# Kernel optimization log

Measured on AMD Instinct MI355X. Metric: run time of the kernel, lower is better.

Reference implementation:

```python
import jax, jax.numpy as jnp
import numpy as np

N, INV, M, K, H = 131072, 256, 256, 64, 512
EPS = 1e-6  # rms norm eps
LN_EPS = 1e-5  # torch LayerNorm default


def setup_inputs() -> dict:
    key = jax.random.key(0)
    ks = jax.random.split(key, 12)
    r = lambda i, shp, s=1.0: jax.random.normal(ks[i], shp, jnp.float32) * s
    return {
        "atomic_embeddings": r(0, (N, INV + 3 * M)),
        "mean_inv": r(1, (INV,)) * 0.1,
        "std_inv": jax.random.uniform(ks[2], (INV,), jnp.float32, 0.5, 1.5),
        "rms_gamma": jnp.ones((M,), jnp.float32),
        "W0": r(3, (M, K)),
        "W1": r(4, (M, K)),
        "W2": r(5, (M, K)),
        "w_cross": r(6, (K, K)),
        "w_dot": r(7, (K, K)),
        "ln_w": jnp.ones((K,), jnp.float32),
        "ln_b": jnp.zeros((K,), jnp.float32),
        "g_w1": r(8, (INV, H)) / np.sqrt(INV),
        "g_b1": jnp.zeros((H,), jnp.float32),
        "g_w2": r(9, (H, K)) / np.sqrt(H),
        "g_b2": jnp.zeros((K,), jnp.float32),
    }


def reference(atomic_embeddings, mean_inv, std_inv, rms_gamma, W0, W1, W2,
              w_cross, w_dot, ln_w, ln_b, g_w1, g_b1, g_w2, g_b2):
    # split invariants (0e scalars come first) / equivariants (1o vectors)
    inv = atomic_embeddings[:, :INV]                       # [N, INV]
    eq = atomic_embeddings[:, INV:].reshape(-1, M, 3)      # [N, M, 3] e3nn (mul, ir) layout

    # rescale invariants
    inv = (inv - mean_inv) / std_inv

    # equivariant RMS layer norm over the M irrep channels (norm-based)
    n2 = jnp.sum(eq * eq, axis=-1)                          # [N, M] squared vector norms
    rms = jnp.sqrt(jnp.mean(n2, axis=-1, keepdims=True) + EPS)  # [N, 1]
    eq = eq * (rms_gamma / rms)[..., None]                  # [N, M, 3]

    # o3.Linear Mx1o -> Kx1o (per-component GEMM, e3nn 1/sqrt(fan_in) path norm)
    s_lin = 1.0 / np.sqrt(M)
    x0 = jnp.einsum('nmi,mk->nki', eq, W0) * s_lin          # [N, K, 3]
    x1 = jnp.einsum('nmi,mk->nki', eq, W1) * s_lin
    x2 = jnp.einsum('nmi,mk->nki', eq, W2) * s_lin

    # tp_cross: Kx1o (x) Kx1o -> Kx1e, 'uvu' weighted, component norm.
    # CG(1,1->1) = eps_ijk/sqrt(6); path weight sqrt(dim(1e)/fan_in)=sqrt(3/K)
    # => overall 1/sqrt(2K). Contract weight into x1 first to stay O(N K^2).
    y1 = jnp.einsum('nvj,uv->nuj', x1, w_cross)             # [N, K, 3]
    cross = jnp.cross(x0, y1) / np.sqrt(2.0 * K)            # [N, K, 3] (1e)

    # tp_dot: Kx1e (x) Kx1o -> Kx0o, 'uvu' weighted, component norm.
    # CG(1,1->0) = delta_ij/sqrt(3); path weight sqrt(1/K) => 1/sqrt(3K).
    y2 = jnp.einsum('nvj,uv->nuj', x2, w_dot)               # [N, K, 3]
    chi = jnp.sum(cross * y2, axis=-1) / np.sqrt(3.0 * K)   # [N, K] pseudoscalars

    # LayerNorm over K
    mu = jnp.mean(chi, axis=-1, keepdims=True)
    var = jnp.mean(jnp.square(chi - mu), axis=-1, keepdims=True)
    out = (chi - mu) / jnp.sqrt(var + LN_EPS) * ln_w + ln_b

    # ChiGate: sigmoid(Linear(SiLU(Linear(inv))))
    gate = jax.nn.sigmoid(jax.nn.silu(inv @ g_w1 + g_b1) @ g_w2 + g_b2)
    return gate * out
```

## Files before the change

kernel.cpp:

```cpp
#include <hip/hip_runtime.h>
#include <math.h>

#define ROW_D 1024
#define INV_D 256

typedef short bf16x8 __attribute__((ext_vector_type(8)));
typedef float f32x4 __attribute__((ext_vector_type(4)));

#define MFMA16(a,b,c) __builtin_amdgcn_mfma_f32_16x16x32_bf16((a),(b),(c),0,0,0)

__device__ __forceinline__ unsigned short f2bf(float f) {
    union { float f; unsigned int u; } x; x.f = f;
    return (unsigned short)((x.u + 0x7FFFu + ((x.u >> 16) & 1u)) >> 16);
}
__device__ __forceinline__ float bf2f(unsigned short h) {
    union { unsigned int u; float f; } x; x.u = ((unsigned int)h) << 16;
    return x.f;
}

__global__ void prep_kernel(
    const float* __restrict__ g_w1, const float* __restrict__ mean_inv,
    const float* __restrict__ std_inv, const float* __restrict__ g_w2,
    const float* __restrict__ W0, const float* __restrict__ W1,
    const float* __restrict__ W2, const float* __restrict__ rms_gamma,
    const float* __restrict__ w_cross, const float* __restrict__ w_dot,
    const float* __restrict__ g_b1,
    unsigned short* __restrict__ W1t, unsigned short* __restrict__ W2t,
    unsigned short* __restrict__ Wcat, unsigned short* __restrict__ wcb,
    unsigned short* __restrict__ wdb, float* __restrict__ b1p)
{
    const int nth = gridDim.x * 256;
    for (int idx = blockIdx.x * 256 + threadIdx.x; idx < 221696; idx += nth) {
        if (idx < 131072) {
            int h = idx >> 8, m = idx & 255;
            W1t[idx] = f2bf(g_w1[m * 512 + h] / std_inv[m]);
        } else if (idx < 163840) {
            int t = idx - 131072; int k = t >> 9, h = t & 511;
            W2t[t] = f2bf(g_w2[h * 64 + k]);
        } else if (idx < 212992) {
            int t = idx - 163840; int r = t >> 8, m = t & 255;
            int tt = r >> 6, k = r & 63;
            const float* Wt = (tt == 0) ? W0 : ((tt == 1) ? W1 : W2);
            Wcat[t] = f2bf(Wt[m * 64 + k] * rms_gamma[m] * 0.0625f);
        } else if (idx < 217088) {
            int t = idx - 212992; wcb[t] = f2bf(w_cross[t]);
        } else if (idx < 221184) {
            int t = idx - 217088; wdb[t] = f2bf(w_dot[t]);
        } else {
            int h = idx - 221184;
            float s = 0.f;
            for (int m = 0; m < 256; ++m)
                s += mean_inv[m] / std_inv[m] * g_w1[m * 512 + h];
            b1p[h] = g_b1[h] - s;
        }
    }
}

__global__ __launch_bounds__(256, 3) void gate_kernel(
    const float* __restrict__ emb,
    const unsigned short* __restrict__ W1t,
    const unsigned short* __restrict__ W2t,
    const float* __restrict__ b1p,
    const float* __restrict__ g_b2,
    float* __restrict__ out)
{
    __shared__ __align__(16) char smem[43008];
    unsigned short* As   = (unsigned short*)smem;
    unsigned short* acts = (unsigned short*)(smem + 33792);

    const int tid = threadIdx.x;
    const int wv = tid >> 6, ln = tid & 63;
    const int lr = ln & 15, lq = ln >> 4;
    const int wr = (wv & 1) << 1;
    const int wc = (wv >> 1) << 1;
    const long n0 = (long)blockIdx.x * 64;

#pragma unroll
    for (int i = 0; i < 16; ++i) {
        int idx = tid + i * 256;
        int atom = idx >> 6;
        int c4 = (idx & 63) << 2;
        float4 v = *(const float4*)(emb + (n0 + atom) * ROW_D + c4);
        ushort4 h;
        h.x = f2bf(v.x); h.y = f2bf(v.y); h.z = f2bf(v.z); h.w = f2bf(v.w);
        *(ushort4*)&As[atom * 264 + c4] = h;
    }
    __syncthreads();

    f32x4 acc2[2][2];
#pragma unroll
    for (int r = 0; r < 2; ++r)
#pragma unroll
        for (int c = 0; c < 2; ++c) acc2[r][c] = (f32x4){0.f, 0.f, 0.f, 0.f};

    for (int hc = 0; hc < 8; ++hc) {
        f32x4 acc1[2][2];
#pragma unroll
        for (int r = 0; r < 2; ++r)
#pragma unroll
            for (int c = 0; c < 2; ++c) acc1[r][c] = (f32x4){0.f, 0.f, 0.f, 0.f};

#pragma unroll
        for (int ks = 0; ks < 8; ++ks) {
            bf16x8 af[2], bf[2];
#pragma unroll
            for (int r = 0; r < 2; ++r)
                af[r] = *(const bf16x8*)&As[((wr + r) * 16 + lr) * 264 + ks * 32 + lq * 8];
#pragma unroll
            for (int c = 0; c < 2; ++c)
                bf[c] = *(const bf16x8*)(W1t + (hc * 64 + (wc + c) * 16 + lr) * 256
                                              + ks * 32 + lq * 8);
#pragma unroll
            for (int r = 0; r < 2; ++r)
#pragma unroll
                for (int c = 0; c < 2; ++c)
                    acc1[r][c] = MFMA16(af[r], bf[c], acc1[r][c]);
        }

#pragma unroll
        for (int c = 0; c < 2; ++c) {
            int hl = (wc + c) * 16 + lr;
            float b = b1p[hc * 64 + hl];
#pragma unroll
            for (int r = 0; r < 2; ++r)
#pragma unroll
                for (int g = 0; g < 4; ++g) {
                    int atom = (wr + r) * 16 + lq * 4 + g;
                    float v = acc1[r][c][g] + b;
                    acts[atom * 72 + hl] = f2bf(v / (1.f + __expf(-v)));
                }
        }
        __syncthreads();

#pragma unroll
        for (int ks = 0; ks < 2; ++ks) {
            bf16x8 af[2], bf[2];
#pragma unroll
            for (int r = 0; r < 2; ++r)
                af[r] = *(const bf16x8*)&acts[((wr + r) * 16 + lr) * 72 + ks * 32 + lq * 8];
#pragma unroll
            for (int c = 0; c < 2; ++c)
                bf[c] = *(const bf16x8*)(W2t + ((wc + c) * 16 + lr) * 512
                                              + hc * 64 + ks * 32 + lq * 8);
#pragma unroll
            for (int r = 0; r < 2; ++r)
#pragma unroll
                for (int c = 0; c < 2; ++c)
                    acc2[r][c] = MFMA16(af[r], bf[c], acc2[r][c]);
        }
        __syncthreads();
    }

#pragma unroll
    for (int c = 0; c < 2; ++c) {
        int k = (wc + c) * 16 + lr;
        float b2v = g_b2[k];
#pragma unroll
        for (int r = 0; r < 2; ++r)
#pragma unroll
            for (int g = 0; g < 4; ++g) {
                int atom = (wr + r) * 16 + lq * 4 + g;
                float v = acc2[r][c][g] + b2v;
                out[(n0 + atom) * 64 + k] = 1.f / (1.f + __expf(-v));
            }
    }
}

__global__ __launch_bounds__(256, 3) void chi_kernel(
    const float* __restrict__ emb,
    const unsigned short* __restrict__ Wcat,
    const unsigned short* __restrict__ wcb,
    const unsigned short* __restrict__ wdb,
    const float* __restrict__ ln_w,
    const float* __restrict__ ln_b,
    float* __restrict__ out)
{
    __shared__ __align__(16) char smem[49024];
    unsigned short* Aeq = (unsigned short*)smem;
    unsigned short* Xl1 = (unsigned short*)smem;
    unsigned short* Xl2 = (unsigned short*)(smem + 13824);
    unsigned short* y1l = (unsigned short*)smem;
    unsigned short* y2l = (unsigned short*)(smem + 13824);
    unsigned short* x0l = (unsigned short*)(smem + 27648);
    float* chi_s = (float*)(smem + 40192);
    float* rms_s = (float*)(smem + 48640);
    float* mu_s  = (float*)(smem + 48768);
    float* isd_s = (float*)(smem + 48896);

    const int tid = threadIdx.x;
    const int wv = tid >> 6, ln = tid & 63;
    const int lr = ln & 15, lq = ln >> 4;
    const int a_t = tid >> 3, st = tid & 7;
    const long n0 = (long)blockIdx.x * 32;

    f32x4 acc[6][3];
#pragma unroll
    for (int tr = 0; tr < 6; ++tr)
#pragma unroll
        for (int c = 0; c < 3; ++c) acc[tr][c] = (f32x4){0.f, 0.f, 0.f, 0.f};
    float sumsq = 0.f;

    for (int half = 0; half < 2; ++half) {
        if (half) __syncthreads();
#pragma unroll
        for (int g = 0; g < 4; ++g) {
            int m0 = st * 16 + g * 4;
            int mg = half * 128 + m0;
            const float* p = emb + (n0 + a_t) * ROW_D + INV_D + (long)mg * 3;
            float4 v0 = *(const float4*)(p);
            float4 v1 = *(const float4*)(p + 4);
            float4 v2 = *(const float4*)(p + 8);
            sumsq += v0.x * v0.x + v0.y * v0.y + v0.z * v0.z + v0.w * v0.w
                   + v1.x * v1.x + v1.y * v1.y + v1.z * v1.z + v1.w * v1.w
                   + v2.x * v2.x + v2.y * v2.y + v2.z * v2.z + v2.w * v2.w;
            ushort4 h0, h1, h2;
            h0.x = f2bf(v0.x); h0.y = f2bf(v0.w); h0.z = f2bf(v1.z); h0.w = f2bf(v2.y);
            h1.x = f2bf(v0.y); h1.y = f2bf(v1.x); h1.z = f2bf(v1.w); h1.w = f2bf(v2.z);
            h2.x = f2bf(v0.z); h2.y = f2bf(v1.y); h2.z = f2bf(v2.x); h2.w = f2bf(v2.w);
            *(ushort4*)&Aeq[(0 * 32 + a_t) * 136 + m0] = h0;
            *(ushort4*)&Aeq[(1 * 32 + a_t) * 136 + m0] = h1;
            *(ushort4*)&Aeq[(2 * 32 + a_t) * 136 + m0] = h2;
        }
        __syncthreads();
#pragma unroll
        for (int ks = 0; ks < 4; ++ks) {
            bf16x8 bfr[3];
#pragma unroll
            for (int c = 0; c < 3; ++c)
                bfr[c] = *(const bf16x8*)(Wcat + ((wv * 3 + c) * 16 + lr) * 256
                                               + half * 128 + ks * 32 + lq * 8);
#pragma unroll
            for (int tr = 0; tr < 6; ++tr) {
                bf16x8 af = *(const bf16x8*)&Aeq[(tr * 16 + lr) * 136 + ks * 32 + lq * 8];
#pragma unroll
                for (int c = 0; c < 3; ++c)
                    acc[tr][c] = MFMA16(af, bfr[c], acc[tr][c]);
            }
        }
    }
    sumsq += __shfl_xor(sumsq, 1);
    sumsq += __shfl_xor(sumsq, 2);
    sumsq += __shfl_xor(sumsq, 4);
    if (st == 0) rms_s[a_t] = rsqrtf(sumsq * (1.f / 256.f) + 1e-6f);
    __syncthreads();

    float rmv[2][4];
#pragma unroll
    for (int p = 0; p < 2; ++p)
#pragma unroll
        for (int g = 0; g < 4; ++g) rmv[p][g] = rms_s[p * 16 + lq * 4 + g];

#pragma unroll
    for (int tr = 0; tr < 6; ++tr)
#pragma unroll
        for (int c = 0; c < 3; ++c) {
            int colg = (wv * 3 + c) * 16 + lr;
            int t = colg >> 6, k = colg & 63;
#pragma unroll
            for (int g = 0; g < 4; ++g) {
                int rowg = tr * 16 + lq * 4 + g;
                int ii = rowg >> 5, atom = rowg & 31;
                unsigned short hb = f2bf(acc[tr][c][g] * rmv[tr & 1][g]);
                if (t == 0)      x0l[atom * 196 + k * 3 + ii] = hb;
                else if (t == 1) Xl1[(atom * 3 + ii) * 72 + k] = hb;
                else             Xl2[(atom * 3 + ii) * 72 + k] = hb;
            }
        }
    __syncthreads();

    const int ts = wv & 1, cp = wv >> 1;
    const unsigned short* Xs = ts ? Xl2 : Xl1;
    const unsigned short* Wg = ts ? wdb : wcb;
    f32x4 yacc[6][2];
#pragma unroll
    for (int tr = 0; tr < 6; ++tr)
#pragma unroll
        for (int c = 0; c < 2; ++c) yacc[tr][c] = (f32x4){0.f, 0.f, 0.f, 0.f};
#pragma unroll
    for (int ks = 0; ks < 2; ++ks) {
        bf16x8 bfr[2];
#pragma unroll
        for (int c = 0; c < 2; ++c)
            bfr[c] = *(const bf16x8*)(Wg + ((cp * 2 + c) * 16 + lr) * 64 + ks * 32 + lq * 8);
#pragma unroll
        for (int tr = 0; tr < 6; ++tr) {
            bf16x8 af = *(const bf16x8*)&Xs[(tr * 16 + lr) * 72 + ks * 32 + lq * 8];
#pragma unroll
            for (int c = 0; c < 2; ++c)
                yacc[tr][c] = MFMA16(af, bfr[c], yacc[tr][c]);
        }
    }
    __syncthreads();

    unsigned short* Yd = ts ? y2l : y1l;
#pragma unroll
    for (int tr = 0; tr < 6; ++tr)
#pragma unroll
        for (int c = 0; c < 2; ++c) {
            int u = (cp * 2 + c) * 16 + lr;
#pragma unroll
            for (int g = 0; g < 4; ++g) {
                int rowg = tr * 16 + lq * 4 + g;
                Yd[rowg * 72 + u] = f2bf(yacc[tr][c][g]);
            }
        }
    __syncthreads();

    const float CHI_SCALE = 1.0f / sqrtf(24576.0f);
#pragma unroll
    for (int q = 0; q < 8; ++q) {
        int u = st + 8 * q;
        float x0a = bf2f(x0l[a_t * 196 + u * 3 + 0]);
        float x0b = bf2f(x0l[a_t * 196 + u * 3 + 1]);
        float x0c = bf2f(x0l[a_t * 196 + u * 3 + 2]);
        float y1a = bf2f(y1l[(a_t * 3 + 0) * 72 + u]);
        float y1b = bf2f(y1l[(a_t * 3 + 1) * 72 + u]);
        float y1c = bf2f(y1l[(a_t * 3 + 2) * 72 + u]);
        float y2a = bf2f(y2l[(a_t * 3 + 0) * 72 + u]);
        float y2b = bf2f(y2l[(a_t * 3 + 1) * 72 + u]);
        float y2c = bf2f(y2l[(a_t * 3 + 2) * 72 + u]);
        float c0 = x0b * y1c - x0c * y1b;
        float c1 = x0c * y1a - x0a * y1c;
        float c2 = x0a * y1b - x0b * y1a;
        chi_s[a_t * 66 + u] = (c0 * y2a + c1 * y2b + c2 * y2c) * CHI_SCALE;
    }
    __syncthreads();

    float s = 0.f;
#pragma unroll
    for (int q = 0; q < 8; ++q) s += chi_s[a_t * 66 + st + 8 * q];
    s += __shfl_xor(s, 1); s += __shfl_xor(s, 2); s += __shfl_xor(s, 4);
    float mu = s * (1.f / 64.f);
    float vv = 0.f;
#pragma unroll
    for (int q = 0; q < 8; ++q) {
        float d = chi_s[a_t * 66 + st + 8 * q] - mu;
        vv += d * d;
    }
    vv += __shfl_xor(vv, 1); vv += __shfl_xor(vv, 2); vv += __shfl_xor(vv, 4);
    if (st == 0) {
        mu_s[a_t]  = mu;
        isd_s[a_t] = rsqrtf(vv * (1.f / 64.f) + 1e-5f);
    }
    __syncthreads();

    float lw = ln_w[ln], lb = ln_b[ln];
#pragma unroll
    for (int aa = 0; aa < 8; ++aa) {
        int atom = wv * 8 + aa;
        float val = (chi_s[atom * 66 + ln] - mu_s[atom]) * isd_s[atom] * lw + lb;
        long o = (n0 + atom) * 64 + ln;
        out[o] = out[o] * val;
    }
}

extern "C" void kernel_launch(void* const* d_in, const int* in_sizes, int n_in,
                              void* d_out, int out_size, void* d_ws, size_t ws_size,
                              hipStream_t stream)
{
    const float* emb       = (const float*)d_in[0];
    const float* mean_inv  = (const float*)d_in[1];
    const float* std_inv   = (const float*)d_in[2];
    const float* rms_gamma = (const float*)d_in[3];
    const float* W0        = (const float*)d_in[4];
    const float* W1        = (const float*)d_in[5];
    const float* W2        = (const float*)d_in[6];
    const float* w_cross   = (const float*)d_in[7];
    const float* w_dot     = (const float*)d_in[8];
    const float* ln_w      = (const float*)d_in[9];
    const float* ln_b      = (const float*)d_in[10];
    const float* g_w1      = (const float*)d_in[11];
    const float* g_b1      = (const float*)d_in[12];
    const float* g_w2      = (const float*)d_in[13];
    const float* g_b2      = (const float*)d_in[14];
    float* out = (float*)d_out;

    char* ws = (char*)d_ws;
    unsigned short* W1t  = (unsigned short*)(ws);
    unsigned short* W2t  = (unsigned short*)(ws + 262144);
    unsigned short* Wcat = (unsigned short*)(ws + 327680);
    unsigned short* wcb  = (unsigned short*)(ws + 425984);
    unsigned short* wdb  = (unsigned short*)(ws + 434176);
    float*          b1p  = (float*)(ws + 442368);

    const int N = in_sizes[0] / ROW_D;

    prep_kernel<<<128, 256, 0, stream>>>(g_w1, mean_inv, std_inv, g_w2,
                                         W0, W1, W2, rms_gamma, w_cross, w_dot,
                                         g_b1, W1t, W2t, Wcat, wcb, wdb, b1p);
    gate_kernel<<<N / 64, 256, 0, stream>>>(emb, W1t, W2t, b1p, g_b2, out);
    chi_kernel<<<N / 32, 256, 0, stream>>>(emb, Wcat, wcb, wdb, ln_w, ln_b, out);
}
```

Measured before the change: 970.4 us.

## Give each wave its own 16-atom tile in gate kernel, keep A in registers

The gate MLP kernel now assigns each wave 16 atoms across all 64 output columns, instead of a 2x2 wave grid sharing a 64-atom tile. The invariant inputs go straight from global memory into registers as bf16 fragments, so the A tile in shared memory and its staging are gone. The SiLU activations go into a per-wave LDS slice, which removes the block-wide barriers. The trade-off is twice as many weight-fragment loads per wave from global/L2 and higher register pressure from holding 8 A fragments.

```diff
diff --git a/kernel.cpp b/kernel.cpp
--- a/kernel.cpp
+++ b/kernel.cpp
@@ -64,105 +64,81 @@
     const float* __restrict__ g_b2,
     float* __restrict__ out)
 {
-    __shared__ __align__(16) char smem[43008];
-    unsigned short* As   = (unsigned short*)smem;
-    unsigned short* acts = (unsigned short*)(smem + 33792);
+    __shared__ __align__(16) unsigned short acts[4][16][72];
 
     const int tid = threadIdx.x;
     const int wv = tid >> 6, ln = tid & 63;
     const int lr = ln & 15, lq = ln >> 4;
-    const int wr = (wv & 1) << 1;
-    const int wc = (wv >> 1) << 1;
-    const long n0 = (long)blockIdx.x * 64;
-
-#pragma unroll
-    for (int i = 0; i < 16; ++i) {
-        int idx = tid + i * 256;
-        int atom = idx >> 6;
-        int c4 = (idx & 63) << 2;
-        float4 v = *(const float4*)(emb + (n0 + atom) * ROW_D + c4);
-        ushort4 h;
-        h.x = f2bf(v.x); h.y = f2bf(v.y); h.z = f2bf(v.z); h.w = f2bf(v.w);
-        *(ushort4*)&As[atom * 264 + c4] = h;
-    }
-    __syncthreads();
-
-    f32x4 acc2[2][2];
-#pragma unroll
-    for (int r = 0; r < 2; ++r)
-#pragma unroll
-        for (int c = 0; c < 2; ++c) acc2[r][c] = (f32x4){0.f, 0.f, 0.f, 0.f};
+    const long n0 = (long)blockIdx.x * 64 + wv * 16;
+
+    bf16x8 af[8];
+    const float* arow = emb + (n0 + lr) * ROW_D;
+#pragma unroll
+    for (int ks = 0; ks < 8; ++ks) {
+        const float* p = arow + ks * 32 + lq * 8;
+        float4 v0 = *(const float4*)(p);
+        float4 v1 = *(const float4*)(p + 4);
+        bf16x8 a;
+        a[0] = f2bf(v0.x); a[1] = f2bf(v0.y); a[2] = f2bf(v0.z); a[3] = f2bf(v0.w);
+        a[4] = f2bf(v1.x); a[5] = f2bf(v1.y); a[6] = f2bf(v1.z); a[7] = f2bf(v1.w);
+        af[ks] = a;
+    }
+
+    f32x4 acc2[4];
+#pragma unroll
+    for (int c = 0; c < 4; ++c) acc2[c] = (f32x4){0.f, 0.f, 0.f, 0.f};
 
     for (int hc = 0; hc < 8; ++hc) {
-        f32x4 acc1[2][2];
-#pragma unroll
-        for (int r = 0; r < 2; ++r)
-#pragma unroll
-            for (int c = 0; c < 2; ++c) acc1[r][c] = (f32x4){0.f, 0.f, 0.f, 0.f};
+        f32x4 acc1[4];
+#pragma unroll
+        for (int c = 0; c < 4; ++c) acc1[c] = (f32x4){0.f, 0.f, 0.f, 0.f};
 
 #pragma unroll
         for (int ks = 0; ks < 8; ++ks) {
-            bf16x8 af[2], bf[2];
-#pragma unroll
-            for (int r = 0; r < 2; ++r)
-                af[r] = *(const bf16x8*)&As[((wr + r) * 16 + lr) * 264 + ks * 32 + lq * 8];
-#pragma unroll
-            for (int c = 0; c < 2; ++c)
-                bf[c] = *(const bf16x8*)(W1t + (hc * 64 + (wc + c) * 16 + lr) * 256
+            bf16x8 bf[4];
+#pragma unroll
+            for (int c = 0; c < 4; ++c)
+                bf[c] = *(const bf16x8*)(W1t + (hc * 64 + c * 16 + lr) * 256
                                               + ks * 32 + lq * 8);
 #pragma unroll
-            for (int r = 0; r < 2; ++r)
-#pragma unroll
-                for (int c = 0; c < 2; ++c)
-                    acc1[r][c] = MFMA16(af[r], bf[c], acc1[r][c]);
-        }
-
-#pragma unroll
-        for (int c = 0; c < 2; ++c) {
-            int hl = (wc + c) * 16 + lr;
+            for (int c = 0; c < 4; ++c)
+                acc1[c] = MFMA16(af[ks], bf[c], acc1[c]);
+        }
+
+#pragma unroll
+        for (int c = 0; c < 4; ++c) {
+            int hl = c * 16 + lr;
             float b = b1p[hc * 64 + hl];
 #pragma unroll
-            for (int r = 0; r < 2; ++r)
-#pragma unroll
-                for (int g = 0; g < 4; ++g) {
-                    int atom = (wr + r) * 16 + lq * 4 + g;
-                    float v = acc1[r][c][g] + b;
-                    acts[atom * 72 + hl] = f2bf(v / (1.f + __expf(-v)));
-                }
-        }
-        __syncthreads();
+            for (int g = 0; g < 4; ++g) {
+                float v = acc1[c][g] + b;
+                acts[wv][lq * 4 + g][hl] = f2bf(v / (1.f + __expf(-v)));
+            }
+        }
 
 #pragma unroll
         for (int ks = 0; ks < 2; ++ks) {
-            bf16x8 af[2], bf[2];
-#pragma unroll
-            for (int r = 0; r < 2; ++r)
-                af[r] = *(const bf16x8*)&acts[((wr + r) * 16 + lr) * 72 + ks * 32 + lq * 8];
-#pragma unroll
-            for (int c = 0; c < 2; ++c)
-                bf[c] = *(const bf16x8*)(W2t + ((wc + c) * 16 + lr) * 512
+            bf16x8 aft = *(const bf16x8*)&acts[wv][lr][ks * 32 + lq * 8];
+            bf16x8 bf[4];
+#pragma unroll
+            for (int c = 0; c < 4; ++c)
+                bf[c] = *(const bf16x8*)(W2t + (c * 16 + lr) * 512
                                               + hc * 64 + ks * 32 + lq * 8);
 #pragma unroll
-            for (int r = 0; r < 2; ++r)
-#pragma unroll
-                for (int c = 0; c < 2; ++c)
-                    acc2[r][c] = MFMA16(af[r], bf[c], acc2[r][c]);
-        }
-        __syncthreads();
-    }
-
-#pragma unroll
-    for (int c = 0; c < 2; ++c) {
-        int k = (wc + c) * 16 + lr;
+            for (int c = 0; c < 4; ++c)
+                acc2[c] = MFMA16(aft, bf[c], acc2[c]);
+        }
+    }
+
+#pragma unroll
+    for (int c = 0; c < 4; ++c) {
+        int k = c * 16 + lr;
         float b2v = g_b2[k];
 #pragma unroll
-        for (int r = 0; r < 2; ++r)
-#pragma unroll
-            for (int g = 0; g < 4; ++g) {
-                int atom = (wr + r) * 16 + lq * 4 + g;
-                float v = acc2[r][c][g] + b2v;
-                out[(n0 + atom) * 64 + k] = 1.f / (1.f + __expf(-v));
-            }
+        for (int g = 0; g < 4; ++g) {
+            float v = acc2[c][g] + b2v;
+            out[(n0 + lq * 4 + g) * 64 + k] = 1.f / (1.f + __expf(-v));
+        }
     }
 }
 
@@ -231,10 +207,10 @@
                                                + half * 128 + ks * 32 + lq * 8);
 #pragma unroll
             for (int tr = 0; tr < 6; ++tr) {
-                bf16x8 af = *(const bf16x8*)&Aeq[(tr * 16 + lr) * 136 + ks * 32 + lq * 8];
+                bf16x8 afr = *(const bf16x8*)&Aeq[(tr * 16 + lr) * 136 + ks * 32 + lq * 8];
 #pragma unroll
                 for (int c = 0; c < 3; ++c)
-                    acc[tr][c] = MFMA16(af, bfr[c], acc[tr][c]);
+                    acc[tr][c] = MFMA16(afr, bfr[c], acc[tr][c]);
             }
         }
     }
@@ -284,10 +260,10 @@
             bfr[c] = *(const bf16x8*)(Wg + ((cp * 2 + c) * 16 + lr) * 64 + ks * 32 + lq * 8);
 #pragma unroll
         for (int tr = 0; tr < 6; ++tr) {
-            bf16x8 af = *(const bf16x8*)&Xs[(tr * 16 + lr) * 72 + ks * 32 + lq * 8];
+            bf16x8 afr = *(const bf16x8*)&Xs[(tr * 16 + lr) * 72 + ks * 32 + lq * 8];
 #pragma unroll
             for (int c = 0; c < 2; ++c)
-                yacc[tr][c] = MFMA16(af, bfr[c], yacc[tr][c]);
+                yacc[tr][c] = MFMA16(afr, bfr[c], yacc[tr][c]);
         }
     }
     __syncthreads();
```

After: 1.094 ms. 1.13x slower.
